# Optimization experiments

Hardware: AMD Instinct MI355X
Metric: run time of the kernel (lower is better)

Reference implementation:

```python
import jax, jax.numpy as jnp
import numpy as np

B, I, H, O, M = 4096, 1024, 2048, 256, 100


def _lin(key, out_dim, in_dim):
    kw, kb = jax.random.split(key)
    s = 1.0 / np.sqrt(in_dim)
    W = jax.random.uniform(kw, (out_dim, in_dim), jnp.float32, -s, s)
    b = jax.random.uniform(kb, (out_dim,), jnp.float32, -s, s)
    return W, b


def setup_inputs() -> dict:
    key = jax.random.key(0)
    ks = jax.random.split(key, 12)
    W_ch2, b_ch2 = _lin(ks[0], H, I + 3 * H)   # combined_to_hidden2
    W_cm2, b_cm2 = _lin(ks[1], M, I + 3 * H)   # combined_to_middle2
    W_mo, b_mo = _lin(ks[2], O, M)             # middle_to_out
    W_ci, b_ci = _lin(ks[3], H, I)             # linear_cell_i
    W_ch, b_ch = _lin(ks[4], H, H)             # linear_cell_h
    W_fc, b_fc = _lin(ks[5], H, H)             # linear_for_cell
    bias = jax.random.normal(ks[6], (H,), jnp.float32)  # self.bias ~ N(0,1)
    return {
        "input": jax.random.normal(ks[7], (B, I), jnp.float32),
        "hidden": jax.random.normal(ks[8], (B, H), jnp.float32),
        "prev_hidden": jax.random.normal(ks[9], (B, H), jnp.float32),
        "cell": jax.random.normal(ks[10], (B, H), jnp.float32),
        "W_ch2": W_ch2, "b_ch2": b_ch2,
        "W_cm2": W_cm2, "b_cm2": b_cm2,
        "W_mo": W_mo, "b_mo": b_mo,
        "W_ci": W_ci, "b_ci": b_ci,
        "W_ch": W_ch, "b_ch": b_ch,
        "W_fc": W_fc, "b_fc": b_fc,
        "bias": bias,
        "k": 1,
    }


def reference(input, hidden, prev_hidden, cell,
              W_ch2, b_ch2, W_cm2, b_cm2, W_mo, b_mo,
              W_ci, b_ci, W_ch, b_ch, W_fc, b_fc, bias, k):
    # k > 0 branch of TEXTnetOrder2.forward (k is a static Python int)
    assert k != 0
    combined = jnp.concatenate([input, hidden, prev_hidden, cell], axis=1)  # [B, I+3H]
    new_hidden = combined @ W_ch2.T + b_ch2                                  # [B, H]
    mid = jax.nn.relu(combined @ W_cm2.T + b_cm2)                            # [B, 100]
    # dropout(p=0.5) is identity in eval mode
    out = mid @ W_mo.T + b_mo                                                # [B, O]
    h_proj = new_hidden @ W_ch.T + b_ch                                      # linear_cell_h(hidden)
    lc = (input @ W_ci.T + b_ci) + h_proj + bias
    new_cell = jnp.tanh(lc @ W_fc.T + b_fc)      # state update (detached in torch)
    new_prev_hidden = h_proj                      # state update (detached in torch)
    return (out, new_hidden, new_cell, new_prev_hidden)
```

## Files before the change

kernel.cpp:

```cpp
#include <hip/hip_runtime.h>
#include <hip/hip_bf16.h>
#include <math.h>

typedef short bf16x8 __attribute__((ext_vector_type(8)));
typedef float f32x4 __attribute__((ext_vector_type(4)));
typedef unsigned short u16;
typedef unsigned short u16x8v __attribute__((ext_vector_type(8)));

#define DEVI __device__ __forceinline__

DEVI u16 f2b(float x) {
  __hip_bfloat16 h = __float2bfloat16(x);
  return *reinterpret_cast<u16*>(&h);
}

DEVI void load_lds16(const void* g, void* l) {
  __builtin_amdgcn_global_load_lds(
      (__attribute__((address_space(1))) void*)(void*)g,
      (__attribute__((address_space(3))) void*)l, 16, 0, 0);
}

DEVI void gemm_core(const u16* __restrict__ A, int lda,
                    const u16* __restrict__ Bw, int ldb,
                    int K, int m0, int n0,
                    u16* As, u16* Bs, f32x4 (&acc)[4][4])
{
  const int tid = threadIdx.x;
  const int w = tid >> 6, l = tid & 63;
  const int wr = w >> 1, wc = w & 1;
  const int lr = l & 15, kg = l >> 4;
  const int c0 = w * 2;
  const int srow = l >> 2, kq = l & 3;

  int aoff[4], boff[4];
#pragma unroll
  for (int m = 0; m < 4; ++m) {
    int ra = wr * 64 + m * 16 + lr;
    aoff[m] = ra * 32 + ((kg ^ ((ra >> 1) & 3)) << 3);
    int rb = wc * 64 + m * 16 + lr;
    boff[m] = rb * 32 + ((kg ^ ((rb >> 1) & 3)) << 3);
  }

  const int row0 = (c0 + 0) * 16 + srow;
  const int row1 = (c0 + 1) * 16 + srow;
  const int kc0 = (kq ^ ((row0 >> 1) & 3)) << 3;
  const int kc1 = (kq ^ ((row1 >> 1) & 3)) << 3;
  const u16* aS0 = A + (long)(m0 + row0) * lda + kc0;
  const u16* aS1 = A + (long)(m0 + row1) * lda + kc1;
  const u16* bS0 = Bw + (long)(n0 + row0) * ldb + kc0;
  const u16* bS1 = Bw + (long)(n0 + row1) * ldb + kc1;
  u16* aD0 = &As[(c0 + 0) * 512];
  u16* aD1 = &As[(c0 + 1) * 512];
  u16* bD0 = &Bs[(c0 + 0) * 512];
  u16* bD1 = &Bs[(c0 + 1) * 512];

  for (int k0 = 0; k0 < K; k0 += 64) {
    __syncthreads();
#pragma unroll
    for (int kh = 0; kh < 2; ++kh) {
      const int gk = k0 + kh * 32;
      const int lk = kh * 4096;
      load_lds16(aS0 + gk, aD0 + lk);
      load_lds16(aS1 + gk, aD1 + lk);
      load_lds16(bS0 + gk, bD0 + lk);
      load_lds16(bS1 + gk, bD1 + lk);
    }
    __syncthreads();

#pragma unroll
    for (int ks = 0; ks < 2; ++ks) {
      bf16x8 af[4], bfr[4];
#pragma unroll
      for (int m = 0; m < 4; ++m)
        af[m] = *reinterpret_cast<const bf16x8*>(&As[ks * 4096 + aoff[m]]);
#pragma unroll
      for (int n = 0; n < 4; ++n)
        bfr[n] = *reinterpret_cast<const bf16x8*>(&Bs[ks * 4096 + boff[n]]);
#pragma unroll
      for (int m = 0; m < 4; ++m)
#pragma unroll
        for (int n = 0; n < 4; ++n)
          acc[m][n] = __builtin_amdgcn_mfma_f32_16x16x32_bf16(af[m], bfr[n], acc[m][n], 0, 0, 0);
    }
  }
}

#define ZERO_ACC(acc) \
  _Pragma("unroll") for (int m = 0; m < 4; ++m) \
  _Pragma("unroll") for (int n = 0; n < 4; ++n) acc[m][n] = (f32x4)0.f;

#define GRID_DECODE(NCOLS) \
  const int xcd = (int)blockIdx.x & 7; \
  const int j = (int)blockIdx.x >> 3; \
  const int bx = j % (NCOLS); \
  const int m0 = (xcd * 4 + j / (NCOLS)) * 128;

#define EPI_VARS() \
  const int tid = threadIdx.x; \
  const int w = tid >> 6, l = tid & 63; \
  const int wr = w >> 1, wc = w & 1; \
  const int lr = l & 15, kg = l >> 4;

__global__ __launch_bounds__(256, 4)
void gemmA(const u16* __restrict__ cmb,
           const u16* __restrict__ wch2b, const float* __restrict__ bch2,
           const u16* __restrict__ wcm2b, const float* __restrict__ bcm2,
           float* __restrict__ out_nh, u16* __restrict__ nhb,
           u16* __restrict__ midb)
{
  __shared__ u16 As[2 * 128 * 32], Bs[2 * 128 * 32];
  GRID_DECODE(17);
  EPI_VARS();
  f32x4 acc[4][4];
  ZERO_ACC(acc);

  if (bx < 16) {
    const int n0 = bx * 128;
    gemm_core(cmb, 7168, wch2b, 7168, 7168, m0, n0, As, Bs, acc);
#pragma unroll
    for (int m = 0; m < 4; ++m) {
      const int r0 = m0 + wr * 64 + m * 16 + kg * 4;
#pragma unroll
      for (int n = 0; n < 4; ++n) {
        const int gc = n0 + wc * 64 + n * 16 + lr;
        const float b1 = bch2[gc];
#pragma unroll
        for (int j2 = 0; j2 < 4; ++j2) {
          const long idx = (long)(r0 + j2) * 2048 + gc;
          float v = acc[m][n][j2] + b1;
          out_nh[idx] = v; nhb[idx] = f2b(v);
        }
      }
    }
  } else {
    gemm_core(cmb, 7168, wcm2b, 7168, 7168, m0, 0, As, Bs, acc);
#pragma unroll
    for (int m = 0; m < 4; ++m) {
      const int r0 = m0 + wr * 64 + m * 16 + kg * 4;
#pragma unroll
      for (int n = 0; n < 4; ++n) {
        const int gc = wc * 64 + n * 16 + lr;
        const float b1 = (gc < 100) ? bcm2[gc] : 0.0f;
#pragma unroll
        for (int j2 = 0; j2 < 4; ++j2) {
          float v = acc[m][n][j2] + b1;
          midb[(long)(r0 + j2) * 128 + gc] = f2b(v > 0.f ? v : 0.f);
        }
      }
    }
  }
}

__global__ __launch_bounds__(256, 4)
void gemmB(const u16* __restrict__ nhb, const u16* __restrict__ wchb,
           const float* __restrict__ bch,
           const u16* __restrict__ cmb, const u16* __restrict__ wcib,
           const float* __restrict__ bci, const float* __restrict__ bias,
           float* __restrict__ out_ph, u16* __restrict__ lcb,
           const u16* __restrict__ midb, const u16* __restrict__ wmob,
           const float* __restrict__ bmo, float* __restrict__ out_out)
{
  __shared__ u16 As[2 * 128 * 32], Bs[2 * 128 * 32];
  GRID_DECODE(18);
  EPI_VARS();
  f32x4 acc[4][4];
  ZERO_ACC(acc);

  if (bx < 16) {
    const int n0 = bx * 128;
    gemm_core(nhb, 2048, wchb, 2048, 2048, m0, n0, As, Bs, acc);
#pragma unroll
    for (int m = 0; m < 4; ++m) {
      const int r0 = m0 + wr * 64 + m * 16 + kg * 4;
#pragma unroll
      for (int n = 0; n < 4; ++n) {
        const int gc = n0 + wc * 64 + n * 16 + lr;
        const float b1 = bch[gc];
#pragma unroll
        for (int j2 = 0; j2 < 4; ++j2)
          out_ph[(long)(r0 + j2) * 2048 + gc] = acc[m][n][j2] + b1;
      }
    }
    gemm_core(cmb, 7168, wcib, 1024, 1024, m0, n0, As, Bs, acc);
#pragma unroll
    for (int m = 0; m < 4; ++m) {
      const int r0 = m0 + wr * 64 + m * 16 + kg * 4;
#pragma unroll
      for (int n = 0; n < 4; ++n) {
        const int gc = n0 + wc * 64 + n * 16 + lr;
        const float b1 = bch[gc] + bci[gc] + bias[gc];
#pragma unroll
        for (int j2 = 0; j2 < 4; ++j2)
          lcb[(long)(r0 + j2) * 2048 + gc] = f2b(acc[m][n][j2] + b1);
      }
    }
  } else {
    const int n0 = (bx - 16) * 128;
    gemm_core(midb, 128, wmob, 128, 128, m0, n0, As, Bs, acc);
#pragma unroll
    for (int m = 0; m < 4; ++m) {
      const int r0 = m0 + wr * 64 + m * 16 + kg * 4;
#pragma unroll
      for (int n = 0; n < 4; ++n) {
        const int gc = n0 + wc * 64 + n * 16 + lr;
        const float b1 = bmo[gc];
#pragma unroll
        for (int j2 = 0; j2 < 4; ++j2)
          out_out[(long)(r0 + j2) * 256 + gc] = acc[m][n][j2] + b1;
      }
    }
  }
}

__global__ __launch_bounds__(256, 4)
void gemmD(const u16* __restrict__ lcb, const u16* __restrict__ wfcb,
           const float* __restrict__ bfc, float* __restrict__ out_cell)
{
  __shared__ u16 As[2 * 128 * 32], Bs[2 * 128 * 32];
  GRID_DECODE(16);
  const int n0 = bx * 128;
  EPI_VARS();
  f32x4 acc[4][4];
  ZERO_ACC(acc);

  gemm_core(lcb, 2048, wfcb, 2048, 2048, m0, n0, As, Bs, acc);
#pragma unroll
  for (int m = 0; m < 4; ++m) {
    const int r0 = m0 + wr * 64 + m * 16 + kg * 4;
#pragma unroll
    for (int n = 0; n < 4; ++n) {
      const int gc = n0 + wc * 64 + n * 16 + lr;
      const float b1 = bfc[gc];
#pragma unroll
      for (int j2 = 0; j2 < 4; ++j2)
        out_cell[(long)(r0 + j2) * 2048 + gc] = tanhf(acc[m][n][j2] + b1);
    }
  }
}

__global__ void cvt_in(const float* __restrict__ x_in, const float* __restrict__ x_hid,
                       const float* __restrict__ x_ph, const float* __restrict__ x_cel,
                       u16* __restrict__ cmb)
{
  const long total = (long)4096 * 896;
  for (long i = blockIdx.x * (long)blockDim.x + threadIdx.x; i < total;
       i += (long)gridDim.x * blockDim.x) {
    const int c8 = (int)(i % 896);
    const long row = i / 896;
    const float* src; long sidx;
    if (c8 < 128)      { src = x_in;  sidx = row * 1024 + (long)c8 * 8; }
    else if (c8 < 384) { src = x_hid; sidx = row * 2048 + (long)(c8 - 128) * 8; }
    else if (c8 < 640) { src = x_ph;  sidx = row * 2048 + (long)(c8 - 384) * 8; }
    else               { src = x_cel; sidx = row * 2048 + (long)(c8 - 640) * 8; }
    float4 v0 = *reinterpret_cast<const float4*>(src + sidx);
    float4 v1 = *reinterpret_cast<const float4*>(src + sidx + 4);
    u16x8v o;
    o[0] = f2b(v0.x); o[1] = f2b(v0.y); o[2] = f2b(v0.z); o[3] = f2b(v0.w);
    o[4] = f2b(v1.x); o[5] = f2b(v1.y); o[6] = f2b(v1.z); o[7] = f2b(v1.w);
    *reinterpret_cast<u16x8v*>(&cmb[row * 7168 + (long)c8 * 8]) = o;
  }
}

__global__ void cvt_w5(const float* __restrict__ s0, const float* __restrict__ s1,
                       const float* __restrict__ s2, const float* __restrict__ s3,
                       const float* __restrict__ s4,
                       u16* __restrict__ d0, u16* __restrict__ d1, u16* __restrict__ d2,
                       u16* __restrict__ d3, u16* __restrict__ d4,
                       long e0, long e1, long e2, long e3, long e4)
{
  for (long i = blockIdx.x * (long)blockDim.x + threadIdx.x; i < e4;
       i += (long)gridDim.x * blockDim.x) {
    const float* s; u16* d; long j;
    if (i < e0)      { s = s0; d = d0; j = i; }
    else if (i < e1) { s = s1; d = d1; j = i - e0; }
    else if (i < e2) { s = s2; d = d2; j = i - e1; }
    else if (i < e3) { s = s3; d = d3; j = i - e2; }
    else             { s = s4; d = d4; j = i - e3; }
    float4 v = reinterpret_cast<const float4*>(s)[j];
    ushort4 o; o.x = f2b(v.x); o.y = f2b(v.y); o.z = f2b(v.z); o.w = f2b(v.w);
    reinterpret_cast<ushort4*>(d)[j] = o;
  }
}

__global__ void cvt_wmo(const float* __restrict__ src, u16* __restrict__ dst)
{
  int i = blockIdx.x * blockDim.x + threadIdx.x;
  if (i < 256 * 100) {
    int r = i / 100, c = i - r * 100;
    dst[r * 128 + c] = f2b(src[i]);
  }
}

extern "C" void kernel_launch(void* const* d_in, const int* in_sizes, int n_in,
                              void* d_out, int out_size, void* d_ws, size_t ws_size,
                              hipStream_t stream) {
  const int B = 4096, I = 1024, H = 2048, O = 256;
  const int K1 = I + 3 * H;

  const float* x_in  = (const float*)d_in[0];
  const float* x_hid = (const float*)d_in[1];
  const float* x_ph  = (const float*)d_in[2];
  const float* x_cel = (const float*)d_in[3];
  const float* Wch2  = (const float*)d_in[4];
  const float* bch2  = (const float*)d_in[5];
  const float* Wcm2  = (const float*)d_in[6];
  const float* bcm2  = (const float*)d_in[7];
  const float* Wmo   = (const float*)d_in[8];
  const float* bmo   = (const float*)d_in[9];
  const float* Wci   = (const float*)d_in[10];
  const float* bci   = (const float*)d_in[11];
  const float* Wch   = (const float*)d_in[12];
  const float* bch   = (const float*)d_in[13];
  const float* Wfc   = (const float*)d_in[14];
  const float* bfc   = (const float*)d_in[15];
  const float* bias  = (const float*)d_in[16];

  float* out_out  = (float*)d_out;
  float* out_nh   = out_out + (long)B * O;
  float* out_cell = out_nh + (long)B * H;
  float* out_ph   = out_cell + (long)B * H;

  char* p = (char*)d_ws;
  u16* cmb   = (u16*)p; p += (long)B * K1 * 2;
  u16* wch2b = (u16*)p; p += (long)H * K1 * 2;
  u16* wcm2b = (u16*)p; p += (long)128 * K1 * 2;
  u16* wmob  = (u16*)p; p += (long)O * 128 * 2;
  u16* wcib  = (u16*)p; p += (long)H * I * 2;
  u16* wchb  = (u16*)p; p += (long)H * H * 2;
  u16* wfcb  = (u16*)p; p += (long)H * H * 2;
  u16* nhb   = (u16*)p; p += (long)B * H * 2;
  u16* midb  = (u16*)p; p += (long)B * 128 * 2;
  u16* lcb   = (u16*)p; p += (long)B * H * 2;

  const dim3 cb(256);

  hipMemsetAsync(wcm2b + (long)100 * K1, 0, (size_t)(28 * K1 + 256 * 128) * 2, stream);

  cvt_in<<<2048, cb, 0, stream>>>(x_in, x_hid, x_ph, x_cel, cmb);
  {
    long e0 = (long)H * K1 / 4;
    long e1 = e0 + (long)100 * K1 / 4;
    long e2 = e1 + (long)H * I / 4;
    long e3 = e2 + (long)H * H / 4;
    long e4 = e3 + (long)H * H / 4;
    cvt_w5<<<2048, cb, 0, stream>>>(Wch2, Wcm2, Wci, Wch, Wfc,
                                    wch2b, wcm2b, wcib, wchb, wfcb,
                                    e0, e1, e2, e3, e4);
  }
  cvt_wmo<<<100, cb, 0, stream>>>(Wmo, wmob);

  gemmA<<<dim3(17 * 32), cb, 0, stream>>>(cmb, wch2b, bch2, wcm2b, bcm2,
                                          out_nh, nhb, midb);
  gemmB<<<dim3(18 * 32), cb, 0, stream>>>(nhb, wchb, bch, cmb, wcib, bci, bias,
                                          out_ph, lcb, midb, wmob, bmo, out_out);
  gemmD<<<dim3(16 * 32), cb, 0, stream>>>(lcb, wfcb, bfc, out_cell);

  (void)in_sizes; (void)n_in; (void)out_size; (void)ws_size;
}
```

Before: 395.2 us.

## Triple-buffer LDS with async prefetch two k-tiles ahead in GEMM core

```diff
diff --git a/kernel.cpp b/kernel.cpp
--- a/kernel.cpp
+++ b/kernel.cpp
@@ -8,6 +8,7 @@
 typedef unsigned short u16x8v __attribute__((ext_vector_type(8)));
 
 #define DEVI __device__ __forceinline__
+#define SCHED_FENCE() __builtin_amdgcn_sched_barrier(0)
 
 DEVI u16 f2b(float x) {
   __hip_bfloat16 h = __float2bfloat16(x);
@@ -23,7 +24,7 @@
 DEVI void gemm_core(const u16* __restrict__ A, int lda,
                     const u16* __restrict__ Bw, int ldb,
                     int K, int m0, int n0,
-                    u16* As, u16* Bs, f32x4 (&acc)[4][4])
+                    u16* lds, f32x4 (&acc)[4][4])
 {
   const int tid = threadIdx.x;
   const int w = tid >> 6, l = tid & 63;
@@ -38,7 +39,7 @@
     int ra = wr * 64 + m * 16 + lr;
     aoff[m] = ra * 32 + ((kg ^ ((ra >> 1) & 3)) << 3);
     int rb = wc * 64 + m * 16 + lr;
-    boff[m] = rb * 32 + ((kg ^ ((rb >> 1) & 3)) << 3);
+    boff[m] = 4096 + rb * 32 + ((kg ^ ((rb >> 1) & 3)) << 3);
   }
 
   const int row0 = (c0 + 0) * 16 + srow;
@@ -49,39 +50,58 @@
   const u16* aS1 = A + (long)(m0 + row1) * lda + kc1;
   const u16* bS0 = Bw + (long)(n0 + row0) * ldb + kc0;
   const u16* bS1 = Bw + (long)(n0 + row1) * ldb + kc1;
-  u16* aD0 = &As[(c0 + 0) * 512];
-  u16* aD1 = &As[(c0 + 1) * 512];
-  u16* bD0 = &Bs[(c0 + 0) * 512];
-  u16* bD1 = &Bs[(c0 + 1) * 512];
-
-  for (int k0 = 0; k0 < K; k0 += 64) {
-    __syncthreads();
-#pragma unroll
-    for (int kh = 0; kh < 2; ++kh) {
-      const int gk = k0 + kh * 32;
-      const int lk = kh * 4096;
-      load_lds16(aS0 + gk, aD0 + lk);
-      load_lds16(aS1 + gk, aD1 + lk);
-      load_lds16(bS0 + gk, bD0 + lk);
-      load_lds16(bS1 + gk, bD1 + lk);
-    }
-    __syncthreads();
-
-#pragma unroll
-    for (int ks = 0; ks < 2; ++ks) {
-      bf16x8 af[4], bfr[4];
-#pragma unroll
-      for (int m = 0; m < 4; ++m)
-        af[m] = *reinterpret_cast<const bf16x8*>(&As[ks * 4096 + aoff[m]]);
+  const int dA0 = (c0 + 0) * 512, dA1 = (c0 + 1) * 512;
+  const int dB0 = 4096 + dA0,     dB1 = 4096 + dA1;
+
+  const int nt = K >> 5;
+
+  auto stage = [&](int t, u16* slot) {
+    const int gk = t * 32;
+    load_lds16(aS0 + gk, slot + dA0);
+    load_lds16(aS1 + gk, slot + dA1);
+    load_lds16(bS0 + gk, slot + dB0);
+    load_lds16(bS1 + gk, slot + dB1);
+  };
+
+  u16* p0 = lds;
+  u16* p1 = lds + 8192;
+  u16* p2 = lds + 16384;
+
+  stage(0, p0);
+  SCHED_FENCE();
+  stage(1, p1);
+  SCHED_FENCE();
+  asm volatile("s_waitcnt vmcnt(4)" ::: "memory");
+  SCHED_FENCE();
+  __builtin_amdgcn_s_barrier();
+  SCHED_FENCE();
+
+  for (int t = 0; t < nt; ++t) {
+    bf16x8 af[4], bfr[4];
+#pragma unroll
+    for (int m = 0; m < 4; ++m)
+      af[m] = *reinterpret_cast<const bf16x8*>(&p0[aoff[m]]);
+#pragma unroll
+    for (int n = 0; n < 4; ++n)
+      bfr[n] = *reinterpret_cast<const bf16x8*>(&p0[boff[n]]);
+
+    const bool pre = (t + 2 < nt);
+    if (pre) stage(t + 2, p2);
+
+#pragma unroll
+    for (int m = 0; m < 4; ++m)
 #pragma unroll
       for (int n = 0; n < 4; ++n)
-        bfr[n] = *reinterpret_cast<const bf16x8*>(&Bs[ks * 4096 + boff[n]]);
-#pragma unroll
-      for (int m = 0; m < 4; ++m)
-#pragma unroll
-        for (int n = 0; n < 4; ++n)
-          acc[m][n] = __builtin_amdgcn_mfma_f32_16x16x32_bf16(af[m], bfr[n], acc[m][n], 0, 0, 0);
-    }
+        acc[m][n] = __builtin_amdgcn_mfma_f32_16x16x32_bf16(af[m], bfr[n], acc[m][n], 0, 0, 0);
+
+    SCHED_FENCE();
+    if (pre) asm volatile("s_waitcnt vmcnt(4)" ::: "memory");
+    else     asm volatile("s_waitcnt vmcnt(0)" ::: "memory");
+    SCHED_FENCE();
+    __builtin_amdgcn_s_barrier();
+    SCHED_FENCE();
+
+    u16* tmp = p0; p0 = p1; p1 = p2; p2 = tmp;
   }
 }
 
@@ -89,11 +109,11 @@
   _Pragma("unroll") for (int m = 0; m < 4; ++m) \
   _Pragma("unroll") for (int n = 0; n < 4; ++n) acc[m][n] = (f32x4)0.f;
 
-#define GRID_DECODE(NCOLS) \
-  const int xcd = (int)blockIdx.x & 7; \
-  const int j = (int)blockIdx.x >> 3; \
-  const int bx = j % (NCOLS); \
-  const int m0 = (xcd * 4 + j / (NCOLS)) * 128;
+#define GRID_DECODE() \
+  const int per = (int)gridDim.x >> 3; \
+  const int id2 = ((int)blockIdx.x & 7) * per + ((int)blockIdx.x >> 3); \
+  const int bx = id2 >> 5; \
+  const int m0 = (id2 & 31) * 128;
 
 #define EPI_VARS() \
   const int tid = threadIdx.x; \
@@ -101,22 +121,22 @@
   const int wr = w >> 1, wc = w & 1; \
   const int lr = l & 15, kg = l >> 4;
 
-__global__ __launch_bounds__(256, 4)
+__global__ __launch_bounds__(256, 3)
 void gemmA(const u16* __restrict__ cmb,
            const u16* __restrict__ wch2b, const float* __restrict__ bch2,
            const u16* __restrict__ wcm2b, const float* __restrict__ bcm2,
            float* __restrict__ out_nh, u16* __restrict__ nhb,
            u16* __restrict__ midb)
 {
-  __shared__ u16 As[2 * 128 * 32], Bs[2 * 128 * 32];
-  GRID_DECODE(17);
+  __shared__ u16 lds[3 * 8192];
+  GRID_DECODE();
   EPI_VARS();
   f32x4 acc[4][4];
   ZERO_ACC(acc);
 
   if (bx < 16) {
     const int n0 = bx * 128;
-    gemm_core(cmb, 7168, wch2b, 7168, 7168, m0, n0, As, Bs, acc);
+    gemm_core(cmb, 7168, wch2b, 7168, 7168, m0, n0, lds, acc);
 #pragma unroll
     for (int m = 0; m < 4; ++m) {
       const int r0 = m0 + wr * 64 + m * 16 + kg * 4;
@@ -133,7 +153,7 @@
       }
     }
   } else {
-    gemm_core(cmb, 7168, wcm2b, 7168, 7168, m0, 0, As, Bs, acc);
+    gemm_core(cmb, 7168, wcm2b, 7168, 7168, m0, 0, lds, acc);
 #pragma unroll
     for (int m = 0; m < 4; ++m) {
       const int r0 = m0 + wr * 64 + m * 16 + kg * 4;
@@ -151,7 +171,7 @@
   }
 }
 
-__global__ __launch_bounds__(256, 4)
+__global__ __launch_bounds__(256, 3)
 void gemmB(const u16* __restrict__ nhb, const u16* __restrict__ wchb,
            const float* __restrict__ bch,
            const u16* __restrict__ cmb, const u16* __restrict__ wcib,
@@ -160,15 +180,15 @@
            const u16* __restrict__ midb, const u16* __restrict__ wmob,
            const float* __restrict__ bmo, float* __restrict__ out_out)
 {
-  __shared__ u16 As[2 * 128 * 32], Bs[2 * 128 * 32];
-  GRID_DECODE(18);
+  __shared__ u16 lds[3 * 8192];
+  GRID_DECODE();
   EPI_VARS();
   f32x4 acc[4][4];
   ZERO_ACC(acc);
 
   if (bx < 16) {
     const int n0 = bx * 128;
-    gemm_core(nhb, 2048, wchb, 2048, 2048, m0, n0, As, Bs, acc);
+    gemm_core(nhb, 2048, wchb, 2048, 2048, m0, n0, lds, acc);
 #pragma unroll
     for (int m = 0; m < 4; ++m) {
       const int r0 = m0 + wr * 64 + m * 16 + kg * 4;
@@ -181,7 +201,7 @@
           out_ph[(long)(r0 + j2) * 2048 + gc] = acc[m][n][j2] + b1;
       }
     }
-    gemm_core(cmb, 7168, wcib, 1024, 1024, m0, n0, As, Bs, acc);
+    gemm_core(cmb, 7168, wcib, 1024, 1024, m0, n0, lds, acc);
 #pragma unroll
     for (int m = 0; m < 4; ++m) {
       const int r0 = m0 + wr * 64 + m * 16 + kg * 4;
@@ -196,7 +216,7 @@
     }
   } else {
     const int n0 = (bx - 16) * 128;
-    gemm_core(midb, 128, wmob, 128, 128, m0, n0, As, Bs, acc);
+    gemm_core(midb, 128, wmob, 128, 128, m0, n0, lds, acc);
 #pragma unroll
     for (int m = 0; m < 4; ++m) {
       const int r0 = m0 + wr * 64 + m * 16 + kg * 4;
@@ -212,18 +232,18 @@
   }
 }
 
-__global__ __launch_bounds__(256, 4)
+__global__ __launch_bounds__(256, 3)
 void gemmD(const u16* __restrict__ lcb, const u16* __restrict__ wfcb,
            const float* __restrict__ bfc, float* __restrict__ out_cell)
 {
-  __shared__ u16 As[2 * 128 * 32], Bs[2 * 128 * 32];
-  GRID_DECODE(16);
+  __shared__ u16 lds[3 * 8192];
+  GRID_DECODE();
   const int n0 = bx * 128;
   EPI_VARS();
   f32x4 acc[4][4];
   ZERO_ACC(acc);
 
-  gemm_core(lcb, 2048, wfcb, 2048, 2048, m0, n0, As, Bs, acc);
+  gemm_core(lcb, 2048, wfcb, 2048, 2048, m0, n0, lds, acc);
 #pragma unroll
   for (int m = 0; m < 4; ++m) {
     const int r0 = m0 + wr * 64 + m * 16 + kg * 4;
```

After: 424.9 us. +7.5%, slower.
